# Performance work log

Measured on AMD Instinct MI355X. Metric: run time of the kernel, lower is better.

The kernel has to match this reference:

```python
import jax, jax.numpy as jnp
import numpy as np

D = 256          # hidden_dim
H = 4            # num_heads
HD = D // H      # head_dim = 64
E = 4            # num_experts (hard-coded in MoE)
TOPK = 2         # top_k (hard-coded)
DFF = 2 * D      # expert ffn width
EPS = 1e-5


def _ln(x, g, b):
    mu = x.mean(-1, keepdims=True)
    var = x.var(-1, keepdims=True)  # biased, matches torch LayerNorm
    return (x - mu) * jax.lax.rsqrt(var + EPS) * g + b


def _ff(x, w1, b1, w2, b2):
    h = jax.nn.gelu(x @ w1 + b1, approximate=False)  # torch nn.GELU default = exact erf
    return h @ w2 + b2


def setup_inputs() -> dict:
    key = jax.random.key(0)
    ks = jax.random.split(key, 24)
    B, S, IN = 4, 2048, 256
    s = 0.02
    inp = {
        'x': jax.random.normal(ks[0], (B, S, IN), jnp.float32),
        'mask': jax.random.randint(ks[1], (B, S), 0, 2).astype(jnp.int32),
        'w_in': jax.random.normal(ks[2], (IN, D), jnp.float32) * s,
        'b_in': jnp.zeros((D,), jnp.float32),
        'g1': jnp.ones((D,), jnp.float32),
        'be1': jnp.zeros((D,), jnp.float32),
        'wq': jax.random.normal(ks[3], (D, D), jnp.float32) * s,
        'bq': jnp.zeros((D,), jnp.float32),
        'wk': jax.random.normal(ks[4], (D, D), jnp.float32) * s,
        'bk': jnp.zeros((D,), jnp.float32),
        'wv': jax.random.normal(ks[5], (D, D), jnp.float32) * s,
        'bv': jnp.zeros((D,), jnp.float32),
        'wo': jax.random.normal(ks[6], (D, D), jnp.float32) * s,
        'bo': jnp.zeros((D,), jnp.float32),
        'g2': jnp.ones((D,), jnp.float32),
        'be2': jnp.zeros((D,), jnp.float32),
        'wg': jax.random.normal(ks[7], (D, E), jnp.float32) * s,
        'bg': jnp.zeros((E,), jnp.float32),
        'ew1': jax.random.normal(ks[8], (E, D, DFF), jnp.float32) * s,
        'eb1': jnp.zeros((E, DFF), jnp.float32),
        'ew2': jax.random.normal(ks[9], (E, DFF, D), jnp.float32) * s,
        'eb2': jnp.zeros((E, D), jnp.float32),
    }
    return inp


def reference(x, mask, w_in, b_in, g1, be1, wq, bq, wk, bk, wv, bv, wo, bo, g2, be2, wg, bg, ew1, eb1, ew2, eb2):
    B, S, _ = x.shape
    x = x @ w_in + b_in
    res = x
    h = _ln(x, g1, be1)
    q = (h @ wq + bq).reshape(B, S, H, HD).transpose(0, 2, 1, 3)  # bhsd
    k = (h @ wk + bk).reshape(B, S, H, HD).transpose(0, 2, 1, 3)
    v = (h @ wv + bv).reshape(B, S, H, HD).transpose(0, 2, 1, 3)
    # RoPE (interleaved pairs, half-concat output, as in source)
    inv_freq = 1.0 / (10000.0 ** (jnp.arange(0, HD, 2, dtype=jnp.float32) / HD))
    ang = jnp.arange(S, dtype=jnp.float32)[:, None] * inv_freq[None, :]  # [S, HD//2]
    sin, cos = jnp.sin(ang), jnp.cos(ang)  # broadcast over (B,H)
    def rot(t):
        ts = t.reshape(B, H, S, HD // 2, 2)
        t0, t1 = ts[..., 0], ts[..., 1]
        return jnp.concatenate([t0 * cos - t1 * sin, t1 * cos + t0 * sin], axis=-1)
    qr, kr = rot(q), rot(k)
    attn = jnp.einsum('bhqd,bhkd->bhqk', qr, kr) * (HD ** -0.5)
    row = mask[:, None, :, None]  # [B,1,S,1] -> masks whole query rows
    attn = jnp.where(row == 0, jnp.float32(-1e4), attn)
    valid = (row * S).astype(jnp.float32)           # [B,1,S,1]
    all_masked = valid == 0
    uniform = jnp.where(row != 0, 1.0 / jnp.maximum(valid, 1.0), 0.0)
    attn = jnp.where(all_masked, uniform, attn)
    attn = jax.nn.softmax(attn, axis=-1)
    out = jnp.einsum('bhqk,bhkd->bhqd', attn, v).transpose(0, 2, 1, 3).reshape(B, S, D)
    out = out @ wo + bo
    x = res + out
    res2 = x
    h2 = _ln(x, g2, be2)
    # MoE (faithful: expert i only applied where top-k slot i picked expert i)
    gp = jax.nn.softmax(h2 @ wg + bg, axis=-1)
    topv, topi = jax.lax.top_k(gp, TOPK)
    moe_out = jnp.zeros_like(h2)
    for i in range(TOPK):
        eo = _ff(h2, ew1[i], eb1[i], ew2[i], eb2[i])
        m = (topi[..., i] == i)[..., None].astype(h2.dtype)
        moe_out = moe_out + m * eo * topv[..., i:i + 1]
    flat = topi.reshape(-1)
    total = sum((flat == i).sum() for i in range(TOPK)).astype(jnp.float32)
    usage = jnp.zeros((E,), jnp.float32) + total
    usage = usage / usage.sum()
    lb = (jnp.std(usage, ddof=1) / usage.mean()) ** 2
    y = res2 + h2  # source discards moe_out / lb (likely a bug); kept live with exact 0* add
    return y + 0.0 * (moe_out.sum() + lb)
```

## Files before the change

### kernel.cpp

```cpp
#include <hip/hip_runtime.h>
#include <cstddef>

#define Bb    4
#define Sq    2048
#define Dd    256
#define Hh    4
#define HDh   64
#define NROWS (Bb*Sq)
#define EPSf  1e-5f

typedef unsigned short u16;
typedef unsigned int   u32;
typedef unsigned long long u64;
typedef __attribute__((ext_vector_type(8))) short  frag_ab;
typedef __attribute__((ext_vector_type(4))) float  frag_cd;

__device__ __forceinline__ u16 f2bf(float f){
    union { float f; u32 u; } v; v.f = f;
    u32 r = v.u + 0x7fffu + ((v.u >> 16) & 1u);
    return (u16)(r >> 16);
}
__device__ __forceinline__ u16 f2bf_trunc(float f){
    union { float f; u32 u; } v; v.f = f;
    return (u16)(v.u >> 16);
}
__device__ __forceinline__ float bf2f(u32 u){
    union { u32 u; float f; } v; v.u = u << 16; return v.f;
}

__global__ __launch_bounds__(256) void k0_prep(
    const float* __restrict__ w_in, const float* __restrict__ wq,
    const float* __restrict__ wk,   const float* __restrict__ wv,
    const float* __restrict__ wo,
    u16* __restrict__ wT, float* __restrict__ tab)
{
    const int bid = blockIdx.x, tid = threadIdx.x;
    if (bid < 80){
        __shared__ float T[64][65];
        const int wsel = bid >> 4, tile = bid & 15;
        const int k0 = (tile >> 2) * 64, n0 = (tile & 3) * 64;
        const float* src = wsel==0 ? w_in : wsel==1 ? wq : wsel==2 ? wk
                         : wsel==3 ? wv : wo;
        #pragma unroll
        for (int i=0;i<16;++i){
            int idx = i*256 + tid, k = idx>>6, n = idx&63;
            T[k][n] = src[(size_t)(k0+k)*Dd + n0 + n];
        }
        __syncthreads();
        u16* dst = wT + (size_t)wsel*Dd*Dd;
        #pragma unroll
        for (int i=0;i<16;++i){
            int idx = i*256 + tid, n = idx>>6, k = idx&63;
            dst[(size_t)(n0+n)*Dd + k0 + k] = f2bf(T[k][n]);
        }
    } else {
        int s = (bid-80)*8 + (tid>>5);
        int p = tid & 31;
        float invf = exp2f(-(float)p * (13.287712379549449f/32.f));
        float sn, cs; sincosf((float)s * invf, &sn, &cs);
        tab[(size_t)s*64 + p]      = cs;
        tab[(size_t)s*64 + 32 + p] = sn;
    }
}

__global__ __launch_bounds__(256) void k1_fused(
    const float* __restrict__ x,  const float* __restrict__ tab,
    const u16* __restrict__ wTin, const u16* __restrict__ wTq,
    const u16* __restrict__ wTk,  const u16* __restrict__ wTv,
    const float* __restrict__ b_in, const float* __restrict__ g1,
    const float* __restrict__ be1,  const float* __restrict__ bq,
    const float* __restrict__ bk,   const float* __restrict__ bv,
    float* __restrict__ x1, u16* __restrict__ qro,
    u16* __restrict__ kro,  u16* __restrict__ vto)
{
    const int tid  = threadIdx.x;
    const int w    = tid >> 6;
    const int lane = tid & 63;
    const int l16  = lane & 15;
    const int quad = lane >> 4;
    const int r0   = blockIdx.x * 16;
    const int b    = r0 >> 11;
    const int s0   = r0 & (Sq-1);
    const int cb   = w * 64;
    const int c4   = cb + quad*4;

    __shared__ u16 Xs[16][264];
    __shared__ u16 Hs[16][264];
    __shared__ u16 Os[16][264];
    __shared__ float red[2][16][4];

    #pragma unroll
    for (int i=0;i<4;++i){
        int f = i*256 + tid;
        int row = f>>6, cc = f&63;
        float4 v4 = *(const float4*)(x + (size_t)(r0+row)*Dd + cc*4);
        u16 pk4[4] = { f2bf(v4.x), f2bf(v4.y), f2bf(v4.z), f2bf(v4.w) };
        *(u64*)&Xs[row][cc*4] = *(u64*)pk4;
    }
    __syncthreads();

    frag_cd acc[4];
    #pragma unroll
    for (int nt=0;nt<4;++nt){
        float4 b4 = *(const float4*)&b_in[c4 + nt*16];
        acc[nt] = (frag_cd){b4.x, b4.y, b4.z, b4.w};
    }
    #pragma unroll
    for (int kc=0;kc<8;++kc){
        frag_ab xa = *(frag_ab*)&Xs[l16][kc*32 + quad*8];
        #pragma unroll
        for (int nt=0;nt<4;++nt){
            frag_ab wf = *(const frag_ab*)&wTin[(size_t)(cb+nt*16+l16)*Dd + kc*32 + quad*8];
            acc[nt] = __builtin_amdgcn_mfma_f32_16x16x32_bf16(wf, xa, acc[nt], 0,0,0);
        }
    }

    float s=0.f, q=0.f;
    #pragma unroll
    for (int nt=0;nt<4;++nt){
        float4 v4 = make_float4(acc[nt][0], acc[nt][1], acc[nt][2], acc[nt][3]);
        *(float4*)&x1[(size_t)(r0+l16)*Dd + c4 + nt*16] = v4;
        s += v4.x+v4.y+v4.z+v4.w;
        q += v4.x*v4.x + v4.y*v4.y + v4.z*v4.z + v4.w*v4.w;
    }
    s += __shfl_xor(s,16); q += __shfl_xor(q,16);
    s += __shfl_xor(s,32); q += __shfl_xor(q,32);
    if (lane < 16){ red[0][l16][w]=s; red[1][l16][w]=q; }
    __syncthreads();

    {
        float mu = (red[0][l16][0]+red[0][l16][1]+red[0][l16][2]+red[0][l16][3])*(1.f/Dd);
        float ms = (red[1][l16][0]+red[1][l16][1]+red[1][l16][2]+red[1][l16][3])*(1.f/Dd);
        float rstd = rsqrtf(ms - mu*mu + EPSf);
        #pragma unroll
        for (int nt=0;nt<4;++nt){
            float4 g4 = *(const float4*)&g1[c4 + nt*16];
            float4 e4 = *(const float4*)&be1[c4 + nt*16];
            u16 pk4[4] = { f2bf((acc[nt][0]-mu)*rstd*g4.x + e4.x),
                           f2bf((acc[nt][1]-mu)*rstd*g4.y + e4.y),
                           f2bf((acc[nt][2]-mu)*rstd*g4.z + e4.z),
                           f2bf((acc[nt][3]-mu)*rstd*g4.w + e4.w) };
            *(u64*)&Hs[l16][c4 + nt*16] = *(u64*)pk4;
        }
    }
    __syncthreads();

    const u16*   wps[3] = { wTq, wTk, wTv };
    const float* bps[3] = { bq, bk, bv };
    #pragma unroll
    for (int tt=0; tt<3; ++tt){
        frag_cd a2[4];
        #pragma unroll
        for (int nt=0;nt<4;++nt){
            float4 b4 = *(const float4*)&bps[tt][c4 + nt*16];
            a2[nt] = (frag_cd){b4.x, b4.y, b4.z, b4.w};
        }
        #pragma unroll
        for (int kc=0;kc<8;++kc){
            frag_ab ha = *(frag_ab*)&Hs[l16][kc*32 + quad*8];
            #pragma unroll
            for (int nt=0;nt<4;++nt){
                frag_ab wf = *(const frag_ab*)&wps[tt][(size_t)(cb+nt*16+l16)*Dd + kc*32 + quad*8];
                a2[nt] = __builtin_amdgcn_mfma_f32_16x16x32_bf16(wf, ha, a2[nt], 0,0,0);
            }
        }
        #pragma unroll
        for (int nt=0;nt<4;++nt){
            u16 pk4[4] = { f2bf(a2[nt][0]), f2bf(a2[nt][1]),
                           f2bf(a2[nt][2]), f2bf(a2[nt][3]) };
            *(u64*)&Os[l16][c4 + nt*16] = *(u64*)pk4;
        }
        __syncthreads();

        if (tt < 2){
            const int row  = tid >> 4;
            const int head = (tid >> 2) & 3;
            const int pq   = tid & 3;
            const int sidx = s0 + row;
            const float* tb = tab + (size_t)sidx*64;
            float4 c0 = *(const float4*)(tb + pq*8);
            float4 c1 = *(const float4*)(tb + pq*8 + 4);
            float4 sn0 = *(const float4*)(tb + 32 + pq*8);
            float4 sn1 = *(const float4*)(tb + 32 + pq*8 + 4);
            const float cA[8] = {c0.x,c0.y,c0.z,c0.w,c1.x,c1.y,c1.z,c1.w};
            const float sA[8] = {sn0.x,sn0.y,sn0.z,sn0.w,sn1.x,sn1.y,sn1.z,sn1.w};
            u16* dst = (tt==0 ? qro : kro) + ((size_t)(b*Hh+head)*Sq + sidx)*HDh;
            u16 lo[8], hi[8];
            #pragma unroll
            for (int j=0;j<8;++j){
                int p = pq*8 + j;
                u32 pr = *(const u32*)&Os[row][head*64 + 2*p];
                float t0 = bf2f(pr & 0xffffu), t1 = bf2f(pr >> 16);
                lo[j] = f2bf(t0*cA[j] - t1*sA[j]);
                hi[j] = f2bf(t1*cA[j] + t0*sA[j]);
            }
            *(float4*)(dst + pq*8)      = *(float4*)lo;
            *(float4*)(dst + 32 + pq*8) = *(float4*)hi;
        } else {
            const int head = tid >> 6, d = tid & 63;
            u16 pk[16];
            #pragma unroll
            for (int j=0;j<16;++j) pk[j] = Os[j][head*64 + d];
            u16* dst = vto + ((size_t)(b*Hh+head)*HDh + d)*Sq + s0;
            *(float4*)dst     = *(float4*)pk;
            *(float4*)(dst+8) = *(float4*)&pk[8];
        }
        __syncthreads();
    }
}

__global__ __launch_bounds__(256) void k2_attn(
    const u16* __restrict__ qr, const u16* __restrict__ kr,
    const u16* __restrict__ vt, const int* __restrict__ mask,
    u16* __restrict__ Opart, float* __restrict__ lpart)
{
    const int tid = threadIdx.x;
    const int w   = tid >> 6;
    const int lane= tid & 63;
    const int l16 = lane & 15;
    const int quad= lane >> 4;
    const int qt  = blockIdx.x;
    const int bh  = blockIdx.y;
    const int ks  = blockIdx.z;
    const int b   = bh >> 2;
    const int q0  = qt * 64;

    __shared__ u16 Qs [64][72];
    __shared__ u16 Ks [64][72];
    __shared__ u16 Vts[64][72];
    __shared__ u16 Ps [4][16][72];

    const u16* qg = qr + ((size_t)bh*Sq + q0)*HDh;
    for (int cc=tid; cc<512; cc+=256){
        int row = cc>>3, part = cc&7;
        *(float4*)&Qs[row][part*8] = *(const float4*)(qg + row*HDh + part*8);
    }
    __syncthreads();

    frag_ab qf0 = *(frag_ab*)&Qs[w*16 + l16][quad*8];
    frag_ab qf1 = *(frag_ab*)&Qs[w*16 + l16][quad*8 + 32];

    const float mf2 = (mask[(size_t)b*Sq + q0 + w*16 + l16] != 0)
                    ? 0.125f*1.44269504f : 0.f;

    float lsum = 0.f;
    frag_cd O[4];
    #pragma unroll
    for (int d=0; d<4; ++d) O[d] = (frag_cd){0.f,0.f,0.f,0.f};

    const u16* kg0 = kr + (size_t)bh*Sq*HDh + (size_t)ks*1024*HDh;
    const u16* vg0 = vt + (size_t)bh*HDh*Sq + (size_t)ks*1024;

    for (int kt=0; kt<16; ++kt){
        __syncthreads();
        const u16* kg = kg0 + (size_t)kt*64*HDh;
        const u16* vg = vg0 + kt*64;
        for (int cc=tid; cc<512; cc+=256){
            int row = cc>>3, part = cc&7;
            *(float4*)&Ks[row][part*8]  = *(const float4*)(kg + row*HDh  + part*8);
            *(float4*)&Vts[row][part*8] = *(const float4*)(vg + (size_t)row*Sq + part*8);
        }
        __syncthreads();

        frag_cd sc[4];
        #pragma unroll
        for (int t=0;t<4;++t){
            frag_ab kf0 = *(frag_ab*)&Ks[t*16 + l16][quad*8];
            frag_ab kf1 = *(frag_ab*)&Ks[t*16 + l16][quad*8 + 32];
            frag_cd z = (frag_cd){0.f,0.f,0.f,0.f};
            z = __builtin_amdgcn_mfma_f32_16x16x32_bf16(kf0, qf0, z, 0,0,0);
            z = __builtin_amdgcn_mfma_f32_16x16x32_bf16(kf1, qf1, z, 0,0,0);
            sc[t] = z;
        }

        #pragma unroll
        for (int t=0;t<4;++t){
            float p0 = exp2f(sc[t][0]*mf2);
            float p1 = exp2f(sc[t][1]*mf2);
            float p2 = exp2f(sc[t][2]*mf2);
            float p3 = exp2f(sc[t][3]*mf2);
            lsum += p0+p1+p2+p3;
            u16 pk4[4] = { f2bf_trunc(p0), f2bf_trunc(p1),
                           f2bf_trunc(p2), f2bf_trunc(p3) };
            *(u64*)&Ps[w][l16][t*16 + quad*4] = *(u64*)pk4;
        }

        frag_ab pf0 = *(frag_ab*)&Ps[w][l16][quad*8];
        frag_ab pf1 = *(frag_ab*)&Ps[w][l16][quad*8 + 32];

        #pragma unroll
        for (int d=0; d<4; ++d){
            frag_ab vf0 = *(frag_ab*)&Vts[d*16 + l16][quad*8];
            frag_ab vf1 = *(frag_ab*)&Vts[d*16 + l16][quad*8 + 32];
            O[d] = __builtin_amdgcn_mfma_f32_16x16x32_bf16(vf0, pf0, O[d], 0,0,0);
            O[d] = __builtin_amdgcn_mfma_f32_16x16x32_bf16(vf1, pf1, O[d], 0,0,0);
        }
    }

    u16* Ob = Opart + (((size_t)ks*16 + bh)*Sq + q0 + w*16 + l16)*HDh;
    #pragma unroll
    for (int dt=0; dt<4; ++dt){
        u16 pk4[4] = { f2bf(O[dt][0]), f2bf(O[dt][1]),
                       f2bf(O[dt][2]), f2bf(O[dt][3]) };
        *(u64*)(Ob + dt*16 + quad*4) = *(u64*)pk4;
    }
    lsum += __shfl_xor(lsum,16);
    lsum += __shfl_xor(lsum,32);
    if (lane < 16)
        lpart[((size_t)ks*16 + bh)*Sq + q0 + w*16 + l16] = lsum;
}

__global__ __launch_bounds__(256) void k3_gemm_ln(
    const u16* __restrict__ Opart, const float* __restrict__ lpart,
    const u16* __restrict__ wTo,
    const float* __restrict__ bo, const float* __restrict__ x1,
    const float* __restrict__ g2, const float* __restrict__ be2,
    float* __restrict__ out)
{
    const int tid  = threadIdx.x;
    const int w    = tid >> 6;
    const int lane = tid & 63;
    const int l16  = lane & 15;
    const int quad = lane >> 4;
    const int r0   = blockIdx.x * 16;
    const int b    = r0 >> 11;
    const int s0   = r0 & (Sq-1);
    const int cb   = w * 64;
    const int c4   = cb + quad*4;

    __shared__ u16 Ats[16][264];
    __shared__ float red[2][16][4];
    __shared__ float linv[4][16];

    if (tid < 64){
        int h = tid >> 4, r = tid & 15;
        size_t li = ((size_t)(b*Hh + h))*Sq + s0 + r;
        linv[h][r] = 1.f / (lpart[li] + lpart[(size_t)16*Sq + li]);
    }
    __syncthreads();

    const size_t SPLIT = (size_t)16*Sq*HDh;
    #pragma unroll
    for (int i=0;i<4;++i){
        int idx = i*256 + tid;
        int h = idx >> 8, rem = idx & 255, row = rem >> 4, c = rem & 15;
        size_t base = (((size_t)(b*Hh + h))*Sq + s0 + row)*HDh + c*4;
        u64 p0 = *(const u64*)(Opart + base);
        u64 p1 = *(const u64*)(Opart + SPLIT + base);
        float li = linv[h][row];
        u16 pk[4];
        #pragma unroll
        for (int j=0;j<4;++j){
            float v0 = bf2f((u32)((p0 >> (16*j)) & 0xffffu));
            float v1 = bf2f((u32)((p1 >> (16*j)) & 0xffffu));
            pk[j] = f2bf((v0+v1)*li);
        }
        *(u64*)&Ats[row][h*64 + c*4] = *(u64*)pk;
    }
    __syncthreads();

    frag_cd acc[4];
    #pragma unroll
    for (int nt=0;nt<4;++nt){
        float4 b4 = *(const float4*)&bo[c4 + nt*16];
        acc[nt] = (frag_cd){b4.x, b4.y, b4.z, b4.w};
    }
    #pragma unroll
    for (int kc=0;kc<8;++kc){
        frag_ab aa = *(frag_ab*)&Ats[l16][kc*32 + quad*8];
        #pragma unroll
        for (int nt=0;nt<4;++nt){
            frag_ab wf = *(const frag_ab*)&wTo[(size_t)(cb+nt*16+l16)*Dd + kc*32 + quad*8];
            acc[nt] = __builtin_amdgcn_mfma_f32_16x16x32_bf16(wf, aa, acc[nt], 0,0,0);
        }
    }

    float s=0.f, q=0.f;
    #pragma unroll
    for (int nt=0;nt<4;++nt){
        float4 r4 = *(const float4*)&x1[(size_t)(r0+l16)*Dd + c4 + nt*16];
        acc[nt][0] += r4.x; acc[nt][1] += r4.y;
        acc[nt][2] += r4.z; acc[nt][3] += r4.w;
        s += acc[nt][0]+acc[nt][1]+acc[nt][2]+acc[nt][3];
        q += acc[nt][0]*acc[nt][0] + acc[nt][1]*acc[nt][1]
           + acc[nt][2]*acc[nt][2] + acc[nt][3]*acc[nt][3];
    }
    s += __shfl_xor(s,16); q += __shfl_xor(q,16);
    s += __shfl_xor(s,32); q += __shfl_xor(q,32);
    if (lane < 16){ red[0][l16][w]=s; red[1][l16][w]=q; }
    __syncthreads();

    {
        float mu = (red[0][l16][0]+red[0][l16][1]+red[0][l16][2]+red[0][l16][3])*(1.f/Dd);
        float ms = (red[1][l16][0]+red[1][l16][1]+red[1][l16][2]+red[1][l16][3])*(1.f/Dd);
        float rstd = rsqrtf(ms - mu*mu + EPSf);
        #pragma unroll
        for (int nt=0;nt<4;++nt){
            float4 g4 = *(const float4*)&g2[c4 + nt*16];
            float4 e4 = *(const float4*)&be2[c4 + nt*16];
            float4 o4;
            o4.x = acc[nt][0] + (acc[nt][0]-mu)*rstd*g4.x + e4.x;
            o4.y = acc[nt][1] + (acc[nt][1]-mu)*rstd*g4.y + e4.y;
            o4.z = acc[nt][2] + (acc[nt][2]-mu)*rstd*g4.z + e4.z;
            o4.w = acc[nt][3] + (acc[nt][3]-mu)*rstd*g4.w + e4.w;
            *(float4*)&out[(size_t)(r0+l16)*Dd + c4 + nt*16] = o4;
        }
    }
}

extern "C" void kernel_launch(void* const* d_in, const int* in_sizes, int n_in,
                              void* d_out, int out_size, void* d_ws, size_t ws_size,
                              hipStream_t stream)
{
    const float* x    = (const float*)d_in[0];
    const int*   mask = (const int*)  d_in[1];
    const float* w_in = (const float*)d_in[2];
    const float* b_in = (const float*)d_in[3];
    const float* g1   = (const float*)d_in[4];
    const float* be1  = (const float*)d_in[5];
    const float* wq   = (const float*)d_in[6];
    const float* bq   = (const float*)d_in[7];
    const float* wk   = (const float*)d_in[8];
    const float* bk   = (const float*)d_in[9];
    const float* wv   = (const float*)d_in[10];
    const float* bv   = (const float*)d_in[11];
    const float* wo   = (const float*)d_in[12];
    const float* bo   = (const float*)d_in[13];
    const float* g2   = (const float*)d_in[14];
    const float* be2  = (const float*)d_in[15];

    float* out = (float*)d_out;
    char*  wsb = (char*)d_ws;

    float* x1    = (float*)(wsb);
    float* tab   = (float*)(wsb + ( 8u<<20));
    u16*   qro   = (u16*)(wsb + (12u<<20));
    u16*   kro   = (u16*)(wsb + (16u<<20));
    u16*   vto   = (u16*)(wsb + (20u<<20));
    u16*   Opart = (u16*)(wsb + (24u<<20));
    float* lpart = (float*)(wsb + (32u<<20));
    u16*   wT    = (u16*)(wsb + (33u<<20));

    k0_prep<<<336, 256, 0, stream>>>(w_in, wq, wk, wv, wo, wT, tab);
    k1_fused<<<NROWS/16, 256, 0, stream>>>(
        x, tab, wT, wT + Dd*Dd, wT + 2*Dd*Dd, wT + 3*Dd*Dd,
        b_in, g1, be1, bq, bk, bv, x1, qro, kro, vto);
    k2_attn<<<dim3(Sq/64, Bb*Hh, 2), 256, 0, stream>>>(qro, kro, vto, mask, Opart, lpart);
    k3_gemm_ln<<<NROWS/16, 256, 0, stream>>>(Opart, lpart, wT + 4*Dd*Dd,
                                             bo, x1, g2, be2, out);
}
```

Before: 193.3 us.

## Enlarge attention query tile to 128 rows and split keys four ways

The attention kernel now handles 128 query rows per block with 8 waves (512 threads). Each wave loads its Q fragments straight from global memory, skipping the shared-memory staging. The key range is split into four chunks of 512 instead of two of 1024, so the grid stays the same size. The output-projection kernel sums four partial outputs and normalisers, and the workspace layout grows to hold them. Each loaded K/V tile now serves twice as many queries, at the cost of doubling the partial-result traffic and the combine work in the final kernel.

New measurement: 189.1 us. 1.02x faster.

```diff
diff --git a/kernel.cpp b/kernel.cpp
--- a/kernel.cpp
+++ b/kernel.cpp
@@ -209,7 +209,7 @@
     }
 }
 
-__global__ __launch_bounds__(256) void k2_attn(
+__global__ __launch_bounds__(512) void k2_attn(
     const u16* __restrict__ qr, const u16* __restrict__ kr,
     const u16* __restrict__ vt, const int* __restrict__ mask,
     u16* __restrict__ Opart, float* __restrict__ lpart)
@@ -223,22 +223,15 @@
     const int bh  = blockIdx.y;
     const int ks  = blockIdx.z;
     const int b   = bh >> 2;
-    const int q0  = qt * 64;
-
-    __shared__ u16 Qs [64][72];
+    const int q0  = qt * 128;
+
     __shared__ u16 Ks [64][72];
     __shared__ u16 Vts[64][72];
-    __shared__ u16 Ps [4][16][72];
-
-    const u16* qg = qr + ((size_t)bh*Sq + q0)*HDh;
-    for (int cc=tid; cc<512; cc+=256){
-        int row = cc>>3, part = cc&7;
-        *(float4*)&Qs[row][part*8] = *(const float4*)(qg + row*HDh + part*8);
-    }
-    __syncthreads();
-
-    frag_ab qf0 = *(frag_ab*)&Qs[w*16 + l16][quad*8];
-    frag_ab qf1 = *(frag_ab*)&Qs[w*16 + l16][quad*8 + 32];
+    __shared__ u16 Ps [8][16][72];
+
+    const u16* qg = qr + ((size_t)bh*Sq + q0 + w*16 + l16)*HDh;
+    frag_ab qf0 = *(const frag_ab*)(qg + quad*8);
+    frag_ab qf1 = *(const frag_ab*)(qg + quad*8 + 32);
 
     const float mf2 = (mask[(size_t)b*Sq + q0 + w*16 + l16] != 0)
                     ? 0.125f*1.44269504f : 0.f;
@@ -248,18 +241,17 @@
     #pragma unroll
     for (int d=0; d<4; ++d) O[d] = (frag_cd){0.f,0.f,0.f,0.f};
 
-    const u16* kg0 = kr + (size_t)bh*Sq*HDh + (size_t)ks*1024*HDh;
-    const u16* vg0 = vt + (size_t)bh*HDh*Sq + (size_t)ks*1024;
-
-    for (int kt=0; kt<16; ++kt){
+    const u16* kg0 = kr + ((size_t)bh*Sq + ks*512)*HDh;
+    const u16* vg0 = vt + (size_t)bh*HDh*Sq + ks*512;
+
+    const int srow = tid >> 3, spart = tid & 7;
+
+    for (int kt=0; kt<8; ++kt){
         __syncthreads();
         const u16* kg = kg0 + (size_t)kt*64*HDh;
         const u16* vg = vg0 + kt*64;
-        for (int cc=tid; cc<512; cc+=256){
-            int row = cc>>3, part = cc&7;
-            *(float4*)&Ks[row][part*8]  = *(const float4*)(kg + row*HDh  + part*8);
-            *(float4*)&Vts[row][part*8] = *(const float4*)(vg + (size_t)row*Sq + part*8);
-        }
+        *(float4*)&Ks [srow][spart*8] = *(const float4*)(kg + srow*HDh + spart*8);
+        *(float4*)&Vts[srow][spart*8] = *(const float4*)(vg + (size_t)srow*Sq + spart*8);
         __syncthreads();
 
         frag_cd sc[4];
@@ -332,10 +324,12 @@
     __shared__ float red[2][16][4];
     __shared__ float linv[4][16];
 
+    const size_t LS = (size_t)16*Sq;
     if (tid < 64){
         int h = tid >> 4, r = tid & 15;
         size_t li = ((size_t)(b*Hh + h))*Sq + s0 + r;
-        linv[h][r] = 1.f / (lpart[li] + lpart[(size_t)16*Sq + li]);
+        linv[h][r] = 1.f / (lpart[li] + lpart[LS + li]
+                          + lpart[2*LS + li] + lpart[3*LS + li]);
     }
     __syncthreads();
 
@@ -347,13 +341,17 @@
         size_t base = (((size_t)(b*Hh + h))*Sq + s0 + row)*HDh + c*4;
         u64 p0 = *(const u64*)(Opart + base);
         u64 p1 = *(const u64*)(Opart + SPLIT + base);
+        u64 p2 = *(const u64*)(Opart + 2*SPLIT + base);
+        u64 p3 = *(const u64*)(Opart + 3*SPLIT + base);
         float li = linv[h][row];
         u16 pk[4];
         #pragma unroll
         for (int j=0;j<4;++j){
-            float v0 = bf2f((u32)((p0 >> (16*j)) & 0xffffu));
-            float v1 = bf2f((u32)((p1 >> (16*j)) & 0xffffu));
-            pk[j] = f2bf((v0+v1)*li);
+            float v = bf2f((u32)((p0 >> (16*j)) & 0xffffu))
+                    + bf2f((u32)((p1 >> (16*j)) & 0xffffu))
+                    + bf2f((u32)((p2 >> (16*j)) & 0xffffu))
+                    + bf2f((u32)((p3 >> (16*j)) & 0xffffu));
+            pk[j] = f2bf(v*li);
         }
         *(u64*)&Ats[row][h*64 + c*4] = *(u64*)pk;
     }
@@ -438,14 +436,14 @@
     u16*   kro   = (u16*)(wsb + (16u<<20));
     u16*   vto   = (u16*)(wsb + (20u<<20));
     u16*   Opart = (u16*)(wsb + (24u<<20));
-    float* lpart = (float*)(wsb + (32u<<20));
-    u16*   wT    = (u16*)(wsb + (33u<<20));
+    float* lpart = (float*)(wsb + (40u<<20));
+    u16*   wT    = (u16*)(wsb + (40u<<20) + (768u<<10));
 
     k0_prep<<<336, 256, 0, stream>>>(w_in, wq, wk, wv, wo, wT, tab);
     k1_fused<<<NROWS/16, 256, 0, stream>>>(
         x, tab, wT, wT + Dd*Dd, wT + 2*Dd*Dd, wT + 3*Dd*Dd,
         b_in, g1, be1, bq, bk, bv, x1, qro, kro, vto);
-    k2_attn<<<dim3(Sq/64, Bb*Hh, 2), 256, 0, stream>>>(qro, kro, vto, mask, Opart, lpart);
+    k2_attn<<<dim3(Sq/128, Bb*Hh, 4), 512, 0, stream>>>(qro, kro, vto, mask, Opart, lpart);
     k3_gemm_ln<<<NROWS/16, 256, 0, stream>>>(Opart, lpart, wT + 4*Dd*Dd,
                                              bo, x1, g2, be2, out);
 }
```
